# Kernel optimization log

Hardware: AMD Instinct MI355X
Metric: run time of the kernel (lower is better)

Reference implementation:

```python
import jax, jax.numpy as jnp
import numpy as np

N_NODES = 100000
N_EDGES = 1600000
D_IN, D_HID, D_OUT = 128, 16, 32


def setup_inputs() -> dict:
    key = jax.random.key(0)
    k1, k2, k3, k4, k5 = jax.random.split(key, 5)
    features = jax.random.normal(k1, (N_NODES, D_IN), dtype=jnp.float32)
    src = jax.random.randint(k2, (N_EDGES,), 0, N_NODES, dtype=jnp.int32)
    dst = jax.random.randint(k3, (N_EDGES,), 0, N_NODES, dtype=jnp.int32)
    # linear layer params (PyTorch Linear: y = x @ W.T + b); store as (in, out)
    s1 = 1.0 / np.sqrt(D_IN)
    s2 = 1.0 / np.sqrt(D_HID)
    W1 = jax.random.uniform(k4, (D_IN, D_HID), minval=-s1, maxval=s1, dtype=jnp.float32)
    b1 = jnp.zeros((D_HID,), dtype=jnp.float32)
    W2 = jax.random.uniform(k5, (D_HID, D_OUT), minval=-s2, maxval=s2, dtype=jnp.float32)
    b2 = jnp.zeros((D_OUT,), dtype=jnp.float32)
    return {"features": features, "src": src, "dst": dst,
            "W1": W1, "b1": b1, "W2": W2, "b2": b2}


def _gcn_layer(h, src, dst, W, b):
    # copy_src + sum: aggregate neighbor (src) features onto dst nodes
    agg = jax.ops.segment_sum(h[src], dst, num_segments=N_NODES)
    return agg @ W + b


def reference(features, src, dst, W1, b1, W2, b2):
    x = jax.nn.relu(_gcn_layer(features, src, dst, W1, b1))
    x = _gcn_layer(x, src, dst, W2, b2)
    return x
```

## Files before the change

### kernel.cpp

```cpp
#include <hip/hip_runtime.h>
#include <hip/hip_bf16.h>

#define N_NODES 100000
#define N_EDGES 1600000
#define D_IN    128
#define D_HID   16
#define D_OUT   32

#define BSHIFT 8
#define BNODES 256
#define NB 391
#define NBPAD 512
#define SCHUNK 4096
#define SBLOCKS 391
#define MMBLOCKS 1563
#define SLAB 4608
#define NOSTRIDE 257

#define SS_HIST   0
#define SS_LBASE  2048
#define SS_GBASE  4096
#define SS_TSCAN  5696
#define SS_SORTED 6720
#define SS_BID    23104
#define SS_BYTES  31296

__device__ inline float bf_lo(unsigned dw) { return __uint_as_float(dw << 16); }
__device__ inline float bf_hi(unsigned dw) { return __uint_as_float(dw & 0xffff0000u); }
__device__ inline unsigned bf_pack(float f0, float f1) {
    union { __hip_bfloat16 h[2]; unsigned u; } pu;
    pu.h[0] = __float2bfloat16(f0);
    pu.h[1] = __float2bfloat16(f1);
    return pu.u;
}
__device__ inline void acc4(float* a, uint2 w) {
    a[0] += bf_lo(w.x); a[1] += bf_hi(w.x);
    a[2] += bf_lo(w.y); a[3] += bf_hi(w.y);
}

__global__ __launch_bounds__(256) void k_fused1(const float* __restrict__ feat,
                                                const float* __restrict__ W1,
                                                const int* __restrict__ src,
                                                const int* __restrict__ dst,
                                                int* __restrict__ cursor,
                                                unsigned* __restrict__ pairs,
                                                unsigned* __restrict__ Yu) {
    __shared__ __align__(16) char smem[SS_BYTES];
    int tid = threadIdx.x, blk = blockIdx.x;

    if (blk < SBLOCKS) {
        int* hist    = (int*)(smem + SS_HIST);
        int* lbase   = (int*)(smem + SS_LBASE);
        int* gbase   = (int*)(smem + SS_GBASE);
        int* tscan   = (int*)(smem + SS_TSCAN);
        unsigned* sorted = (unsigned*)(smem + SS_SORTED);
        unsigned short* bId = (unsigned short*)(smem + SS_BID);

        int base = blk * SCHUNK;
        int nval = N_EDGES - base;
        if (nval > SCHUNK) nval = SCHUNK;

        for (int i = tid; i < NBPAD; i += 256) hist[i] = 0;
        __syncthreads();

        int varr[16], barr[16];
#pragma unroll
        for (int k = 0; k < 16; ++k) {
            int e = base + k * 256 + tid;
            if (e < N_EDGES) {
                int s = src[e], d = dst[e];
                varr[k] = (s << BSHIFT) | (d & (BNODES - 1));
                int b = d >> BSHIFT;
                barr[k] = b;
                atomicAdd(&hist[b], 1);
            } else {
                barr[k] = -1;
            }
        }
        __syncthreads();

        int i0 = tid * 2;
        int h0 = hist[i0], h1 = hist[i0 + 1];
        int lsum = h0 + h1;
        tscan[tid] = lsum;
        __syncthreads();
#pragma unroll
        for (int off = 1; off < 256; off <<= 1) {
            int x = (tid >= off) ? tscan[tid - off] : 0;
            __syncthreads();
            tscan[tid] += x;
            __syncthreads();
        }
        int excl = tscan[tid] - lsum;
        lbase[i0 + 0] = excl;
        lbase[i0 + 1] = excl + h0;
        __syncthreads();

        for (int i = tid; i < NB; i += 256) {
            int c = hist[i];
            if (c > 0) gbase[i] = i * SLAB + atomicAdd(&cursor[i], c);
        }
        __syncthreads();
        for (int i = tid; i < NBPAD; i += 256) hist[i] = 0;
        __syncthreads();

#pragma unroll
        for (int k = 0; k < 16; ++k) {
            int b = barr[k];
            if (b >= 0) {
                int r = atomicAdd(&hist[b], 1);
                int p = lbase[b] + r;
                sorted[p] = (unsigned)varr[k];
                bId[p] = (unsigned short)b;
            }
        }
        __syncthreads();

        for (int i = tid; i < nval; i += 256) {
            int b = bId[i];
            pairs[gbase[b] + (i - lbase[b])] = sorted[i];
        }
    } else {
        float* sW = (float*)smem;
        for (int i = tid; i < D_IN * D_HID; i += 256) sW[i] = W1[i];
        __syncthreads();

        int gid = (blk - SBLOCKS) * 256 + tid;
        int n = gid >> 2;
        int jq = gid & 3;
        if (n >= N_NODES) return;

        const float4* f4 = (const float4*)(feat + (size_t)n * D_IN);
        const float4* sW4 = (const float4*)sW;

        float4 acc = make_float4(0.f, 0.f, 0.f, 0.f);
#pragma unroll 8
        for (int kq = 0; kq < 32; ++kq) {
            float4 f = f4[kq];
            int k0 = kq * 4;
            float4 w0 = sW4[(k0 + 0) * 4 + jq];
            float4 w1 = sW4[(k0 + 1) * 4 + jq];
            float4 w2 = sW4[(k0 + 2) * 4 + jq];
            float4 w3 = sW4[(k0 + 3) * 4 + jq];
            acc.x += f.x * w0.x + f.y * w1.x + f.z * w2.x + f.w * w3.x;
            acc.y += f.x * w0.y + f.y * w1.y + f.z * w2.y + f.w * w3.y;
            acc.z += f.x * w0.z + f.y * w1.z + f.z * w2.z + f.w * w3.z;
            acc.w += f.x * w0.w + f.y * w1.w + f.z * w2.w + f.w * w3.w;
        }
        uint2 o;
        o.x = bf_pack(acc.x, acc.y);
        o.y = bf_pack(acc.z, acc.w);
        ((uint2*)(Yu + (size_t)n * 8))[jq] = o;
    }
}

__global__ __launch_bounds__(1024) void k_sortagg1(const int* __restrict__ cursor,
                                                   unsigned* __restrict__ pairs,
                                                   const uint2* __restrict__ Yu2,
                                                   const float* __restrict__ bias1,
                                                   uint2* __restrict__ H1u2,
                                                   int* __restrict__ node_off) {
    __shared__ unsigned buf[SLAB];
    __shared__ int hist[BNODES];
    __shared__ int lbase[BNODES];
    __shared__ int cur[BNODES];
    __shared__ int t[BNODES];
    __shared__ float sB[D_HID];

    int tid = threadIdx.x, b = blockIdx.x;
    int beg = b * SLAB;
    int cnt = cursor[b];

    if (tid < BNODES) hist[tid] = 0;
    if (tid < D_HID) sB[tid] = bias1[tid];
    __syncthreads();

    for (int i = tid; i < cnt; i += 1024) {
        unsigned p = pairs[beg + i];
        buf[i] = p;
        atomicAdd(&hist[p & (BNODES - 1)], 1);
    }
    __syncthreads();

    if (tid < BNODES) t[tid] = hist[tid];
    __syncthreads();
#pragma unroll
    for (int off = 1; off < BNODES; off <<= 1) {
        int x = 0;
        if (tid < BNODES && tid >= off) x = t[tid - off];
        __syncthreads();
        if (tid < BNODES) t[tid] += x;
        __syncthreads();
    }
    if (tid < BNODES) {
        int excl = t[tid] - hist[tid];
        lbase[tid] = excl;
        cur[tid] = excl;
        node_off[b * NOSTRIDE + tid] = beg + excl;
        if (tid == 0) node_off[b * NOSTRIDE + BNODES] = beg + cnt;
    }
    __syncthreads();

    for (int i = tid; i < cnt; i += 1024) {
        unsigned p = buf[i];
        int pos = atomicAdd(&cur[p & (BNODES - 1)], 1);
        pairs[beg + pos] = p >> BSHIFT;
    }
    __syncthreads();

    int g = tid >> 2, c = tid & 3;
    int n = b * BNODES + g;
    if (n >= N_NODES) return;
    int i = beg + lbase[g];
    int e = beg + cur[g];
    const unsigned* csr = pairs;

    float a[4] = {0.f, 0.f, 0.f, 0.f}, bb[4] = {0.f, 0.f, 0.f, 0.f};
    for (; i + 7 < e; i += 8) {
        unsigned s0 = csr[i],     s1 = csr[i + 1], s2 = csr[i + 2], s3 = csr[i + 3];
        unsigned s4 = csr[i + 4], s5 = csr[i + 5], s6 = csr[i + 6], s7 = csr[i + 7];
        uint2 w0 = Yu2[(size_t)s0 * 4 + c];
        uint2 w1 = Yu2[(size_t)s1 * 4 + c];
        uint2 w2 = Yu2[(size_t)s2 * 4 + c];
        uint2 w3 = Yu2[(size_t)s3 * 4 + c];
        uint2 w4 = Yu2[(size_t)s4 * 4 + c];
        uint2 w5 = Yu2[(size_t)s5 * 4 + c];
        uint2 w6 = Yu2[(size_t)s6 * 4 + c];
        uint2 w7 = Yu2[(size_t)s7 * 4 + c];
        acc4(a, w0); acc4(bb, w1); acc4(a, w2); acc4(bb, w3);
        acc4(a, w4); acc4(bb, w5); acc4(a, w6); acc4(bb, w7);
    }
    for (; i + 3 < e; i += 4) {
        unsigned s0 = csr[i], s1 = csr[i + 1], s2 = csr[i + 2], s3 = csr[i + 3];
        uint2 w0 = Yu2[(size_t)s0 * 4 + c];
        uint2 w1 = Yu2[(size_t)s1 * 4 + c];
        uint2 w2 = Yu2[(size_t)s2 * 4 + c];
        uint2 w3 = Yu2[(size_t)s3 * 4 + c];
        acc4(a, w0); acc4(bb, w1); acc4(a, w2); acc4(bb, w3);
    }
    for (; i < e; ++i) {
        uint2 w = Yu2[(size_t)csr[i] * 4 + c];
        acc4(a, w);
    }
    float f0 = a[0] + bb[0] + sB[c * 4 + 0];
    float f1 = a[1] + bb[1] + sB[c * 4 + 1];
    float f2 = a[2] + bb[2] + sB[c * 4 + 2];
    float f3 = a[3] + bb[3] + sB[c * 4 + 3];
    uint2 o;
    o.x = bf_pack(fmaxf(f0, 0.f), fmaxf(f1, 0.f));
    o.y = bf_pack(fmaxf(f2, 0.f), fmaxf(f3, 0.f));
    H1u2[(size_t)n * 4 + c] = o;
}

__global__ __launch_bounds__(256) void k_agg2(const int* __restrict__ node_off,
                                              const unsigned* __restrict__ csr,
                                              const uint2* __restrict__ H1u2,
                                              const float* __restrict__ W2,
                                              const float* __restrict__ b2,
                                              float* __restrict__ out) {
    __shared__ float sacc[64][D_HID + 1];
    __shared__ float sW2[D_HID * D_OUT];
    __shared__ float sb2[D_OUT];
    int tid = threadIdx.x;
    for (int i2 = tid; i2 < D_HID * D_OUT; i2 += 256) sW2[i2] = W2[i2];
    if (tid < D_OUT) sb2[tid] = b2[tid];

    int g = tid >> 2, c = tid & 3;
    int n = blockIdx.x * 64 + g;

    float a[4] = {0.f, 0.f, 0.f, 0.f}, bb[4] = {0.f, 0.f, 0.f, 0.f};
    if (n < N_NODES) {
        int idx = n + (n >> 8);
        int i = node_off[idx], e = node_off[idx + 1];
        for (; i + 7 < e; i += 8) {
            unsigned s0 = csr[i],     s1 = csr[i + 1], s2 = csr[i + 2], s3 = csr[i + 3];
            unsigned s4 = csr[i + 4], s5 = csr[i + 5], s6 = csr[i + 6], s7 = csr[i + 7];
            uint2 w0 = H1u2[(size_t)s0 * 4 + c];
            uint2 w1 = H1u2[(size_t)s1 * 4 + c];
            uint2 w2 = H1u2[(size_t)s2 * 4 + c];
            uint2 w3 = H1u2[(size_t)s3 * 4 + c];
            uint2 w4 = H1u2[(size_t)s4 * 4 + c];
            uint2 w5 = H1u2[(size_t)s5 * 4 + c];
            uint2 w6 = H1u2[(size_t)s6 * 4 + c];
            uint2 w7 = H1u2[(size_t)s7 * 4 + c];
            acc4(a, w0); acc4(bb, w1); acc4(a, w2); acc4(bb, w3);
            acc4(a, w4); acc4(bb, w5); acc4(a, w6); acc4(bb, w7);
        }
        for (; i + 3 < e; i += 4) {
            unsigned s0 = csr[i], s1 = csr[i + 1], s2 = csr[i + 2], s3 = csr[i + 3];
            uint2 w0 = H1u2[(size_t)s0 * 4 + c];
            uint2 w1 = H1u2[(size_t)s1 * 4 + c];
            uint2 w2 = H1u2[(size_t)s2 * 4 + c];
            uint2 w3 = H1u2[(size_t)s3 * 4 + c];
            acc4(a, w0); acc4(bb, w1); acc4(a, w2); acc4(bb, w3);
        }
        for (; i < e; ++i) {
            uint2 w = H1u2[(size_t)csr[i] * 4 + c];
            acc4(a, w);
        }
    }
    sacc[g][c * 4 + 0] = a[0] + bb[0];
    sacc[g][c * 4 + 1] = a[1] + bb[1];
    sacc[g][c * 4 + 2] = a[2] + bb[2];
    sacc[g][c * 4 + 3] = a[3] + bb[3];
    __syncthreads();

    for (int t2 = tid; t2 < 64 * D_OUT; t2 += 256) {
        int gg = t2 >> 5, o = t2 & 31;
        int node = blockIdx.x * 64 + gg;
        if (node < N_NODES) {
            float acc = sb2[o];
#pragma unroll
            for (int j = 0; j < D_HID; ++j)
                acc = fmaf(sacc[gg][j], sW2[j * D_OUT + o], acc);
            out[(size_t)node * D_OUT + o] = acc;
        }
    }
}

extern "C" void kernel_launch(void* const* d_in, const int* in_sizes, int n_in,
                              void* d_out, int out_size, void* d_ws, size_t ws_size,
                              hipStream_t stream) {
    const float* feat = (const float*)d_in[0];
    const int*   src  = (const int*)d_in[1];
    const int*   dst  = (const int*)d_in[2];
    const float* W1   = (const float*)d_in[3];
    const float* b1   = (const float*)d_in[4];
    const float* W2   = (const float*)d_in[5];
    const float* b2   = (const float*)d_in[6];
    float* out = (float*)d_out;

    char* base = (char*)d_ws;
    unsigned* pairs    = (unsigned*)(base);
    unsigned* Yu       = (unsigned*)(base + 7208960);
    unsigned* H1u      = (unsigned*)(base + 10408960);
    int*      cursor   = (int*)(base + 13608960);
    int*      node_off = (int*)(base + 13613056);

    hipMemsetAsync(cursor, 0, NB * sizeof(int), stream);

    k_fused1   <<<SBLOCKS + MMBLOCKS, 256, 0, stream>>>(feat, W1, src, dst,
                                                        cursor, pairs, Yu);
    k_sortagg1 <<<NB, 1024, 0, stream>>>(cursor, pairs, (const uint2*)Yu, b1,
                                         (uint2*)H1u, node_off);
    k_agg2     <<<(N_NODES + 63) / 64, 256, 0, stream>>>(node_off, pairs,
                                                         (const uint2*)H1u, W2, b2, out);
}
```

Before: 83.71 us.

## Keep sorted edge slab in LDS for layer-1 gather and layer-2 aggregation

In the sort-aggregate kernel, the locally sorted source indices go into a shared-memory buffer and are written back to global memory coalesced. The layer-1 gather then reads indices from LDS instead of re-reading them from global. The second aggregation kernel changes to one 1024-thread block per 256-node bucket: it stages the whole bucket's index slab and offsets in LDS before gathering. This drops scattered global index writes and repeated global index reads, but doubles LDS use per block and cuts the layer-2 grid from 1563 small blocks to 391 large ones, which may reduce occupancy and latency hiding.

```diff
diff --git a/kernel.cpp b/kernel.cpp
--- a/kernel.cpp
+++ b/kernel.cpp
@@ -161,6 +161,7 @@
                                                    uint2* __restrict__ H1u2,
                                                    int* __restrict__ node_off) {
     __shared__ unsigned buf[SLAB];
+    __shared__ unsigned sbuf[SLAB];
     __shared__ int hist[BNODES];
     __shared__ int lbase[BNODES];
     __shared__ int cur[BNODES];
@@ -204,21 +205,23 @@
     for (int i = tid; i < cnt; i += 1024) {
         unsigned p = buf[i];
         int pos = atomicAdd(&cur[p & (BNODES - 1)], 1);
-        pairs[beg + pos] = p >> BSHIFT;
-    }
-    __syncthreads();
+        sbuf[pos] = p >> BSHIFT;
+    }
+    __syncthreads();
+
+    for (int i = tid; i < cnt; i += 1024)
+        pairs[beg + i] = sbuf[i];
 
     int g = tid >> 2, c = tid & 3;
     int n = b * BNODES + g;
     if (n >= N_NODES) return;
-    int i = beg + lbase[g];
-    int e = beg + cur[g];
-    const unsigned* csr = pairs;
+    int i = lbase[g];
+    int e = cur[g];
 
     float a[4] = {0.f, 0.f, 0.f, 0.f}, bb[4] = {0.f, 0.f, 0.f, 0.f};
     for (; i + 7 < e; i += 8) {
-        unsigned s0 = csr[i],     s1 = csr[i + 1], s2 = csr[i + 2], s3 = csr[i + 3];
-        unsigned s4 = csr[i + 4], s5 = csr[i + 5], s6 = csr[i + 6], s7 = csr[i + 7];
+        unsigned s0 = sbuf[i],     s1 = sbuf[i + 1], s2 = sbuf[i + 2], s3 = sbuf[i + 3];
+        unsigned s4 = sbuf[i + 4], s5 = sbuf[i + 5], s6 = sbuf[i + 6], s7 = sbuf[i + 7];
         uint2 w0 = Yu2[(size_t)s0 * 4 + c];
         uint2 w1 = Yu2[(size_t)s1 * 4 + c];
         uint2 w2 = Yu2[(size_t)s2 * 4 + c];
@@ -231,7 +234,7 @@
         acc4(a, w4); acc4(bb, w5); acc4(a, w6); acc4(bb, w7);
     }
     for (; i + 3 < e; i += 4) {
-        unsigned s0 = csr[i], s1 = csr[i + 1], s2 = csr[i + 2], s3 = csr[i + 3];
+        unsigned s0 = sbuf[i], s1 = sbuf[i + 1], s2 = sbuf[i + 2], s3 = sbuf[i + 3];
         uint2 w0 = Yu2[(size_t)s0 * 4 + c];
         uint2 w1 = Yu2[(size_t)s1 * 4 + c];
         uint2 w2 = Yu2[(size_t)s2 * 4 + c];
@@ -239,7 +242,7 @@
         acc4(a, w0); acc4(bb, w1); acc4(a, w2); acc4(bb, w3);
     }
     for (; i < e; ++i) {
-        uint2 w = Yu2[(size_t)csr[i] * 4 + c];
+        uint2 w = Yu2[(size_t)sbuf[i] * 4 + c];
         acc4(a, w);
     }
     float f0 = a[0] + bb[0] + sB[c * 4 + 0];
@@ -252,29 +255,37 @@
     H1u2[(size_t)n * 4 + c] = o;
 }
 
-__global__ __launch_bounds__(256) void k_agg2(const int* __restrict__ node_off,
-                                              const unsigned* __restrict__ csr,
-                                              const uint2* __restrict__ H1u2,
-                                              const float* __restrict__ W2,
-                                              const float* __restrict__ b2,
-                                              float* __restrict__ out) {
-    __shared__ float sacc[64][D_HID + 1];
+__global__ __launch_bounds__(1024) void k_agg2(const int* __restrict__ node_off,
+                                               const unsigned* __restrict__ csr,
+                                               const uint2* __restrict__ H1u2,
+                                               const float* __restrict__ W2,
+                                               const float* __restrict__ b2,
+                                               float* __restrict__ out) {
+    __shared__ unsigned sidx[SLAB];
+    __shared__ int nb[BNODES + 1];
+    __shared__ float sacc[BNODES][D_HID + 1];
     __shared__ float sW2[D_HID * D_OUT];
     __shared__ float sb2[D_OUT];
-    int tid = threadIdx.x;
-    for (int i2 = tid; i2 < D_HID * D_OUT; i2 += 256) sW2[i2] = W2[i2];
+
+    int tid = threadIdx.x, b = blockIdx.x;
+    int beg = b * SLAB;
+    for (int i = tid; i < D_HID * D_OUT; i += 1024) sW2[i] = W2[i];
     if (tid < D_OUT) sb2[tid] = b2[tid];
+    if (tid <= BNODES) nb[tid] = node_off[b * NOSTRIDE + tid];
+    __syncthreads();
+
+    int cnt = nb[BNODES] - beg;
+    for (int i = tid; i < cnt; i += 1024) sidx[i] = csr[beg + i];
+    __syncthreads();
 
     int g = tid >> 2, c = tid & 3;
-    int n = blockIdx.x * 64 + g;
-
+    int n = b * BNODES + g;
     float a[4] = {0.f, 0.f, 0.f, 0.f}, bb[4] = {0.f, 0.f, 0.f, 0.f};
     if (n < N_NODES) {
-        int idx = n + (n >> 8);
-        int i = node_off[idx], e = node_off[idx + 1];
+        int i = nb[g] - beg, e = nb[g + 1] - beg;
         for (; i + 7 < e; i += 8) {
-            unsigned s0 = csr[i],     s1 = csr[i + 1], s2 = csr[i + 2], s3 = csr[i + 3];
-            unsigned s4 = csr[i + 4], s5 = csr[i + 5], s6 = csr[i + 6], s7 = csr[i + 7];
+            unsigned s0 = sidx[i],     s1 = sidx[i + 1], s2 = sidx[i + 2], s3 = sidx[i + 3];
+            unsigned s4 = sidx[i + 4], s5 = sidx[i + 5], s6 = sidx[i + 6], s7 = sidx[i + 7];
             uint2 w0 = H1u2[(size_t)s0 * 4 + c];
             uint2 w1 = H1u2[(size_t)s1 * 4 + c];
             uint2 w2 = H1u2[(size_t)s2 * 4 + c];
@@ -287,7 +298,7 @@
             acc4(a, w4); acc4(bb, w5); acc4(a, w6); acc4(bb, w7);
         }
         for (; i + 3 < e; i += 4) {
-            unsigned s0 = csr[i], s1 = csr[i + 1], s2 = csr[i + 2], s3 = csr[i + 3];
+            unsigned s0 = sidx[i], s1 = sidx[i + 1], s2 = sidx[i + 2], s3 = sidx[i + 3];
             uint2 w0 = H1u2[(size_t)s0 * 4 + c];
             uint2 w1 = H1u2[(size_t)s1 * 4 + c];
             uint2 w2 = H1u2[(size_t)s2 * 4 + c];
@@ -295,7 +306,7 @@
             acc4(a, w0); acc4(bb, w1); acc4(a, w2); acc4(bb, w3);
         }
         for (; i < e; ++i) {
-            uint2 w = H1u2[(size_t)csr[i] * 4 + c];
+            uint2 w = H1u2[(size_t)sidx[i] * 4 + c];
             acc4(a, w);
         }
     }
@@ -305,9 +316,9 @@
     sacc[g][c * 4 + 3] = a[3] + bb[3];
     __syncthreads();
 
-    for (int t2 = tid; t2 < 64 * D_OUT; t2 += 256) {
+    for (int t2 = tid; t2 < BNODES * D_OUT; t2 += 1024) {
         int gg = t2 >> 5, o = t2 & 31;
-        int node = blockIdx.x * 64 + gg;
+        int node = b * BNODES + gg;
         if (node < N_NODES) {
             float acc = sb2[o];
 #pragma unroll
@@ -343,6 +354,6 @@
                                                         cursor, pairs, Yu);
     k_sortagg1 <<<NB, 1024, 0, stream>>>(cursor, pairs, (const uint2*)Yu, b1,
                                          (uint2*)H1u, node_off);
-    k_agg2     <<<(N_NODES + 63) / 64, 256, 0, stream>>>(node_off, pairs,
-                                                         (const uint2*)H1u, W2, b2, out);
-}
+    k_agg2     <<<NB, 1024, 0, stream>>>(node_off, pairs, (const uint2*)H1u,
+                                         W2, b2, out);
+}
```

Result: faster. 75.79 us (-9.5%).
